# Optimization experiments

Hardware: AMD Instinct MI355X
Metric: run time of the kernel (lower is better)

The kernel has to match this reference:

```python
import jax, jax.numpy as jnp
import numpy as np

B, N, D, E = 8, 512, 256, 16384  # batch, num_nodes, hidden_dim, num_edges


def setup_inputs() -> dict:
    key = jax.random.key(0)
    kf, ke, k1, k2, k3, k4 = jax.random.split(key, 6)
    features = jax.random.normal(kf, (B, N, D), dtype=jnp.float32)
    edge_index = jax.random.randint(ke, (2, E), 0, N, dtype=jnp.int64)
    # weight_net: Linear(2D -> D), ReLU, Linear(D -> 1), Sigmoid
    s1 = 1.0 / np.sqrt(2 * D)
    s2 = 1.0 / np.sqrt(D)
    W1 = jax.random.uniform(k1, (2 * D, D), jnp.float32, -s1, s1)
    b1 = jax.random.uniform(k2, (D,), jnp.float32, -s1, s1)
    W2 = jax.random.uniform(k3, (D, 1), jnp.float32, -s2, s2)
    b2 = jax.random.uniform(k4, (1,), jnp.float32, -s2, s2)
    return {"features": features, "W1": W1, "b1": b1, "W2": W2, "b2": b2,
            "edge_index": edge_index}


def reference(features, W1, b1, W2, b2, edge_index):
    src, dst = edge_index[0], edge_index[1]            # [E], [E]
    fi = features[:, src]                              # [B, E, D]
    fj = features[:, dst]                              # [B, E, D]
    pair = jnp.concatenate([fi, fj], axis=-1)          # [B, E, 2D]
    h = jax.nn.relu(jnp.einsum('bef,fh->beh', pair, W1) + b1)   # [B, E, D]
    s = jax.nn.sigmoid(jnp.einsum('beh,ho->beo', h, W2) + b2)[..., 0]  # [B, E]
    bsz, n = features.shape[0], features.shape[1]
    weights = jnp.zeros((bsz, n, n), features.dtype).at[:, src, dst].set(s)
    return weights
```

## Files before the change

kernel.cpp:

```cpp
#include <hip/hip_runtime.h>
#include <hip/hip_bf16.h>
#include <cstdint>

#define B_ 8
#define N_ 512
#define D_ 256
#define E_ 16384
#define H_ 256

#define SA_STRIDE 56
#define SB_STRIDE 56

using bf16x8 = __attribute__((ext_vector_type(8))) short;
using f32x4  = __attribute__((ext_vector_type(4))) float;

__device__ inline unsigned short f2bf(float f) {
    union { float f; unsigned u; } v; v.f = f;
    unsigned u = v.u;
    return (unsigned short)((u + 0x7fffu + ((u >> 16) & 1u)) >> 16);
}

__global__ __launch_bounds__(256)
void prep_k(const float* __restrict__ W1, unsigned short* __restrict__ W1T) {
    __shared__ float tile[64][65];
    const int tb = blockIdx.x, t = threadIdx.x;
    const int h   = tb >> 4;
    const int rem = tb & 15;
    const int tk  = (rem >> 2) * 64;
    const int tn  = (rem & 3) * 64;
    const float* Wh = W1 + (size_t)h * 256 * 256;
    const int c = t & 63, r0 = t >> 6;
#pragma unroll
    for (int i = 0; i < 16; i++) {
        int r = r0 + i * 4;
        tile[r][c] = Wh[(size_t)(tk + r) * 256 + tn + c];
    }
    __syncthreads();
#pragma unroll
    for (int i = 0; i < 16; i++) {
        int rn = r0 + i * 4;
        W1T[(size_t)(h * 256 + tn + rn) * 256 + tk + c] = f2bf(tile[c][rn]);
    }
}

__global__ __launch_bounds__(256)
void node_gemm(const float* __restrict__ feat,
               const unsigned short* __restrict__ W1T,
               unsigned short* __restrict__ P,
               float4* __restrict__ out4) {
    __shared__ unsigned short sA[64 * SA_STRIDE];
    __shared__ unsigned short sB[256 * SB_STRIDE];

    const int t  = threadIdx.x;
    const int bm = blockIdx.x >> 1;
    const int bn = blockIdx.x & 1;
    const int m0 = bm * 64;

    {
        float4 z = make_float4(0.f, 0.f, 0.f, 0.f);
        float4* oz = out4 + (size_t)blockIdx.x * 4096 + t;
#pragma unroll
        for (int i = 0; i < 16; i++) oz[i * 256] = z;
    }

    const int arow = t >> 2;
    const int akg  = (t & 3) * 8;
    const float* pA = feat + (size_t)(m0 + arow) * 256;
    const unsigned short* pB = W1T + (size_t)(bn * 256 + t) * 256;

    const int wave = t >> 6, lane = t & 63, l15 = lane & 15, quad = lane >> 4;

    f32x4 acc[4][4];
#pragma unroll
    for (int rm = 0; rm < 4; rm++)
#pragma unroll
        for (int cn = 0; cn < 4; cn++)
            acc[rm][cn] = (f32x4){0.f, 0.f, 0.f, 0.f};

    for (int k0 = 0; k0 < 256; k0 += 32) {
        __syncthreads();
        {
            float4 lo = *(const float4*)(pA + k0 + akg);
            float4 hi = *(const float4*)(pA + k0 + akg + 4);
            union { bf16x8 v; unsigned short s[8]; } u;
            u.s[0] = f2bf(lo.x); u.s[1] = f2bf(lo.y); u.s[2] = f2bf(lo.z); u.s[3] = f2bf(lo.w);
            u.s[4] = f2bf(hi.x); u.s[5] = f2bf(hi.y); u.s[6] = f2bf(hi.z); u.s[7] = f2bf(hi.w);
            *(bf16x8*)(sA + arow * SA_STRIDE + akg) = u.v;
        }
        {
            const unsigned short* p = pB + k0;
            uint4 q0 = *(const uint4*)(p);
            uint4 q1 = *(const uint4*)(p + 8);
            uint4 q2 = *(const uint4*)(p + 16);
            uint4 q3 = *(const uint4*)(p + 24);
            *(uint4*)(sB + t * SB_STRIDE +  0) = q0;
            *(uint4*)(sB + t * SB_STRIDE +  8) = q1;
            *(uint4*)(sB + t * SB_STRIDE + 16) = q2;
            *(uint4*)(sB + t * SB_STRIDE + 24) = q3;
        }
        __syncthreads();

        bf16x8 af[4], bfr[4];
#pragma unroll
        for (int rm = 0; rm < 4; rm++)
            af[rm] = *(const bf16x8*)(sA + (rm * 16 + l15) * SA_STRIDE + quad * 8);
#pragma unroll
        for (int cn = 0; cn < 4; cn++)
            bfr[cn] = *(const bf16x8*)(sB + (wave * 64 + cn * 16 + l15) * SB_STRIDE + quad * 8);
#pragma unroll
        for (int rm = 0; rm < 4; rm++)
#pragma unroll
            for (int cn = 0; cn < 4; cn++)
                acc[rm][cn] = __builtin_amdgcn_mfma_f32_16x16x32_bf16(af[rm], bfr[cn], acc[rm][cn], 0, 0, 0);
    }

#pragma unroll
    for (int rm = 0; rm < 4; rm++)
#pragma unroll
        for (int cn = 0; cn < 4; cn++) {
            int col = bn * 256 + wave * 64 + cn * 16 + l15;
#pragma unroll
            for (int r = 0; r < 4; r++) {
                int row = m0 + rm * 16 + quad * 4 + r;
                P[(size_t)row * 512 + col] = f2bf(acc[rm][cn][r]);
            }
        }
}

__device__ inline float dot8(uint4 qu, uint4 qv, const float* b1p, const float* w2p) {
    unsigned us[4] = {qu.x, qu.y, qu.z, qu.w};
    unsigned vs[4] = {qv.x, qv.y, qv.z, qv.w};
    float p = 0.f;
#pragma unroll
    for (int j = 0; j < 4; j++) {
        float ulo = __uint_as_float(us[j] << 16);
        float uhi = __uint_as_float(us[j] & 0xffff0000u);
        float vlo = __uint_as_float(vs[j] << 16);
        float vhi = __uint_as_float(vs[j] & 0xffff0000u);
        float hlo = fmaxf(ulo + vlo + b1p[2 * j],     0.f);
        float hhi = fmaxf(uhi + vhi + b1p[2 * j + 1], 0.f);
        p = fmaf(hlo, w2p[2 * j],     p);
        p = fmaf(hhi, w2p[2 * j + 1], p);
    }
    return p;
}

__global__ __launch_bounds__(256)
void edge_score(const unsigned short* __restrict__ P,
                const float* __restrict__ b1, const float* __restrict__ W2,
                const float* __restrict__ b2, const int* __restrict__ eidx,
                float* __restrict__ out) {
    const int b    = blockIdx.x & 7;
    const int blk  = blockIdx.x >> 3;
    const int wave = threadIdx.x >> 6;
    const int lane = threadIdx.x & 63;
    const int g    = lane >> 4;
    const int w    = lane & 15;
    const int e0   = (blk * 4 + wave) * 16;

    float b1r[16], w2r[16];
#pragma unroll
    for (int j = 0; j < 4; j++) {
        *(float4*)(b1r + 4 * j) = *(const float4*)(b1 + w * 16 + 4 * j);
        *(float4*)(w2r + 4 * j) = *(const float4*)(W2 + w * 16 + 4 * j);
    }
    const float b2v = b2[0];

    const unsigned short* Pb = P + (size_t)b * 512 * 512;
    float* outb = out + (size_t)b * 512 * 512;

    int my_e = 0;
    if (lane < 16)      my_e = eidx[e0 + lane];
    else if (lane < 32) my_e = eidx[E_ + e0 + (lane - 16)];

#pragma unroll
    for (int i = 0; i < 4; i++) {
        int eid = i * 4 + g;
        int src = __shfl(my_e, eid);
        int dst = __shfl(my_e, 16 + eid);
        const unsigned short* pu = Pb + (size_t)src * 512 + w * 16;
        const unsigned short* pv = Pb + (size_t)dst * 512 + 256 + w * 16;
        uint4 u0 = *(const uint4*)(pu);
        uint4 u1 = *(const uint4*)(pu + 8);
        uint4 v0 = *(const uint4*)(pv);
        uint4 v1 = *(const uint4*)(pv + 8);
        float p = dot8(u0, v0, b1r, w2r) + dot8(u1, v1, b1r + 8, w2r + 8);
        p += __shfl_xor(p, 1);
        p += __shfl_xor(p, 2);
        p += __shfl_xor(p, 4);
        p += __shfl_xor(p, 8);
        if (w == 0) {
            float s = 1.0f / (1.0f + __expf(-(p + b2v)));
            outb[(size_t)src * 512 + dst] = s;
        }
    }
}

extern "C" void kernel_launch(void* const* d_in, const int* in_sizes, int n_in,
                              void* d_out, int out_size, void* d_ws, size_t ws_size,
                              hipStream_t stream) {
    const float* feat = (const float*)d_in[0];
    const float* W1   = (const float*)d_in[1];
    const float* b1   = (const float*)d_in[2];
    const float* W2   = (const float*)d_in[3];
    const float* b2   = (const float*)d_in[4];
    const int*   eidx = (const int*)d_in[5];
    float* out = (float*)d_out;

    unsigned short* W1T = (unsigned short*)d_ws;
    unsigned short* P   = (unsigned short*)((char*)d_ws + (1 << 20));

    prep_k<<<32, 256, 0, stream>>>(W1, W1T);
    node_gemm<<<128, 256, 0, stream>>>(feat, W1T, P, (float4*)out);
    edge_score<<<2048, 256, 0, stream>>>(P, b1, W2, b2, eidx, out);
}
```

Measured before the change: 92.82 us.

## Sort edges by source and reuse source rows in edge scoring

```diff
diff --git a/kernel.cpp b/kernel.cpp
--- a/kernel.cpp
+++ b/kernel.cpp
@@ -21,31 +21,80 @@
 }
 
 __global__ __launch_bounds__(256)
-void prep_k(const float* __restrict__ W1, unsigned short* __restrict__ W1T) {
+void prep_k(const float* __restrict__ W1, const int* __restrict__ eidx,
+            unsigned short* __restrict__ W1T,
+            int* __restrict__ gStarts, int* __restrict__ gSorted) {
     __shared__ float tile[64][65];
+    __shared__ int hist[4][512];
+    __shared__ int sc[2][512];
+    __shared__ int cursor[512];
+
     const int tb = blockIdx.x, t = threadIdx.x;
-    const int h   = tb >> 4;
-    const int rem = tb & 15;
-    const int tk  = (rem >> 2) * 64;
-    const int tn  = (rem & 3) * 64;
-    const float* Wh = W1 + (size_t)h * 256 * 256;
-    const int c = t & 63, r0 = t >> 6;
-#pragma unroll
-    for (int i = 0; i < 16; i++) {
-        int r = r0 + i * 4;
-        tile[r][c] = Wh[(size_t)(tk + r) * 256 + tn + c];
-    }
-    __syncthreads();
-#pragma unroll
-    for (int i = 0; i < 16; i++) {
-        int rn = r0 + i * 4;
-        W1T[(size_t)(h * 256 + tn + rn) * 256 + tk + c] = f2bf(tile[c][rn]);
+
+    if (tb < 32) {
+        const int h   = tb >> 4;
+        const int rem = tb & 15;
+        const int tk  = (rem >> 2) * 64;
+        const int tn  = (rem & 3) * 64;
+        const float* Wh = W1 + (size_t)h * 256 * 256;
+        const int c = t & 63, r0 = t >> 6;
+#pragma unroll
+        for (int i = 0; i < 16; i++) {
+            int r = r0 + i * 4;
+            tile[r][c] = Wh[(size_t)(tk + r) * 256 + tn + c];
+        }
+        __syncthreads();
+#pragma unroll
+        for (int i = 0; i < 16; i++) {
+            int rn = r0 + i * 4;
+            W1T[(size_t)(h * 256 + tn + rn) * 256 + tk + c] = f2bf(tile[c][rn]);
+        }
+        return;
+    }
+
+    const int w = t >> 6;
+    for (int i = t; i < 4 * 512; i += 256) ((int*)hist)[i] = 0;
+    __syncthreads();
+    for (int i = 0; i < 64; i++) {
+        int s = eidx[t + 256 * i];
+        atomicAdd(&hist[w][s], 1);
+    }
+    __syncthreads();
+    for (int i = t; i < 512; i += 256)
+        sc[0][i] = hist[0][i] + hist[1][i] + hist[2][i] + hist[3][i];
+    __syncthreads();
+    int cur = 0;
+    for (int off = 1; off < 512; off <<= 1) {
+#pragma unroll
+        for (int k = 0; k < 2; k++) {
+            int i = t + 256 * k;
+            int v = sc[cur][i];
+            if (i >= off) v += sc[cur][i - off];
+            sc[cur ^ 1][i] = v;
+        }
+        __syncthreads();
+        cur ^= 1;
+    }
+    for (int i = t; i < 512; i += 256) {
+        int st = (i == 0) ? 0 : sc[cur][i - 1];
+        cursor[i]  = st;
+        gStarts[i] = st;
+    }
+    if (t == 0) gStarts[512] = E_;
+    __syncthreads();
+    for (int i = 0; i < 64; i++) {
+        int e = t + 256 * i;
+        int s = eidx[e];
+        int d = eidx[E_ + e];
+        int pos = atomicAdd(&cursor[s], 1);
+        gSorted[pos] = d;
     }
 }
 
 __global__ __launch_bounds__(256)
 void node_gemm(const float* __restrict__ feat,
                const unsigned short* __restrict__ W1T,
+               const float* __restrict__ b1,
                unsigned short* __restrict__ P,
                float4* __restrict__ out4) {
     __shared__ unsigned short sA[64 * SA_STRIDE];
@@ -115,19 +164,21 @@
     }
 
 #pragma unroll
-    for (int rm = 0; rm < 4; rm++)
-#pragma unroll
-        for (int cn = 0; cn < 4; cn++) {
-            int col = bn * 256 + wave * 64 + cn * 16 + l15;
+    for (int cn = 0; cn < 4; cn++) {
+        int colh = wave * 64 + cn * 16 + l15;
+        float bias = (bn == 0) ? b1[colh] : 0.f;
+        int col = bn * 256 + colh;
+#pragma unroll
+        for (int rm = 0; rm < 4; rm++)
 #pragma unroll
             for (int r = 0; r < 4; r++) {
                 int row = m0 + rm * 16 + quad * 4 + r;
-                P[(size_t)row * 512 + col] = f2bf(acc[rm][cn][r]);
+                P[(size_t)row * 512 + col] = f2bf(acc[rm][cn][r] + bias);
             }
-        }
-}
-
-__device__ inline float dot8(uint4 qu, uint4 qv, const float* b1p, const float* w2p) {
+    }
+}
+
+__device__ inline float dot8nb(uint4 qu, uint4 qv, const float* w2p) {
     unsigned us[4] = {qu.x, qu.y, qu.z, qu.w};
     unsigned vs[4] = {qv.x, qv.y, qv.z, qv.w};
     float p = 0.f;
@@ -137,8 +188,8 @@
         float uhi = __uint_as_float(us[j] & 0xffff0000u);
         float vlo = __uint_as_float(vs[j] << 16);
         float vhi = __uint_as_float(vs[j] & 0xffff0000u);
-        float hlo = fmaxf(ulo + vlo + b1p[2 * j],     0.f);
-        float hhi = fmaxf(uhi + vhi + b1p[2 * j + 1], 0.f);
+        float hlo = fmaxf(ulo + vlo, 0.f);
+        float hhi = fmaxf(uhi + vhi, 0.f);
         p = fmaf(hlo, w2p[2 * j],     p);
         p = fmaf(hhi, w2p[2 * j + 1], p);
     }
@@ -147,52 +198,58 @@
 
 __global__ __launch_bounds__(256)
 void edge_score(const unsigned short* __restrict__ P,
-                const float* __restrict__ b1, const float* __restrict__ W2,
-                const float* __restrict__ b2, const int* __restrict__ eidx,
+                const float* __restrict__ W2, const float* __restrict__ b2,
+                const int* __restrict__ gStarts, const int* __restrict__ gSorted,
                 float* __restrict__ out) {
-    const int b    = blockIdx.x & 7;
-    const int blk  = blockIdx.x >> 3;
-    const int wave = threadIdx.x >> 6;
-    const int lane = threadIdx.x & 63;
-    const int g    = lane >> 4;
-    const int w    = lane & 15;
-    const int e0   = (blk * 4 + wave) * 16;
-
-    float b1r[16], w2r[16];
-#pragma unroll
-    for (int j = 0; j < 4; j++) {
-        *(float4*)(b1r + 4 * j) = *(const float4*)(b1 + w * 16 + 4 * j);
+    const int b     = blockIdx.x & 7;
+    const int chunk = blockIdx.x >> 3;
+    const int lane  = threadIdx.x & 63;
+    const int wave  = threadIdx.x >> 6;
+    const int g     = lane >> 4;
+    const int w     = lane & 15;
+    const int wid   = wave * 4 + g;
+    const int s     = 2 * chunk + (wid >> 3);
+    const int o     = wid & 7;
+
+    const int st = gStarts[s], en = gStarts[s + 1];
+
+    float w2r[16];
+#pragma unroll
+    for (int j = 0; j < 4; j++)
         *(float4*)(w2r + 4 * j) = *(const float4*)(W2 + w * 16 + 4 * j);
-    }
     const float b2v = b2[0];
 
-    const unsigned short* Pb = P + (size_t)b * 512 * 512;
-    float* outb = out + (size_t)b * 512 * 512;
-
-    int my_e = 0;
-    if (lane < 16)      my_e = eidx[e0 + lane];
-    else if (lane < 32) my_e = eidx[E_ + e0 + (lane - 16)];
-
-#pragma unroll
-    for (int i = 0; i < 4; i++) {
-        int eid = i * 4 + g;
-        int src = __shfl(my_e, eid);
-        int dst = __shfl(my_e, 16 + eid);
-        const unsigned short* pu = Pb + (size_t)src * 512 + w * 16;
-        const unsigned short* pv = Pb + (size_t)dst * 512 + 256 + w * 16;
-        uint4 u0 = *(const uint4*)(pu);
-        uint4 u1 = *(const uint4*)(pu + 8);
-        uint4 v0 = *(const uint4*)(pv);
-        uint4 v1 = *(const uint4*)(pv + 8);
-        float p = dot8(u0, v0, b1r, w2r) + dot8(u1, v1, b1r + 8, w2r + 8);
+    const unsigned short* Pu = P + ((size_t)b * 512 + s) * 512 + w * 16;
+    uint4 u0 = *(const uint4*)(Pu);
+    uint4 u1 = *(const uint4*)(Pu + 8);
+    const unsigned short* Pv = P + (size_t)b * 512 * 512 + 256 + w * 16;
+    float* outb = out + ((size_t)b * 512 + s) * 512;
+
+    int j = st + o;
+    int dst0 = 0; uint4 v00 = {}, v01 = {};
+    if (j < en) {
+        dst0 = gSorted[j];
+        const unsigned short* pv = Pv + (size_t)dst0 * 512;
+        v00 = *(const uint4*)pv; v01 = *(const uint4*)(pv + 8);
+    }
+    while (j < en) {
+        int jn = j + 8;
+        int dst1 = 0; uint4 v10 = {}, v11 = {};
+        if (jn < en) {
+            dst1 = gSorted[jn];
+            const unsigned short* pv = Pv + (size_t)dst1 * 512;
+            v10 = *(const uint4*)pv; v11 = *(const uint4*)(pv + 8);
+        }
+        float p = dot8nb(u0, v00, w2r) + dot8nb(u1, v01, w2r + 8);
         p += __shfl_xor(p, 1);
         p += __shfl_xor(p, 2);
         p += __shfl_xor(p, 4);
         p += __shfl_xor(p, 8);
         if (w == 0) {
-            float s = 1.0f / (1.0f + __expf(-(p + b2v)));
-            outb[(size_t)src * 512 + dst] = s;
-        }
+            float sv = 1.0f / (1.0f + __expf(-(p + b2v)));
+            outb[dst0] = sv;
+        }
+        dst0 = dst1; v00 = v10; v01 = v11; j = jn;
     }
 }
 
@@ -209,8 +266,10 @@
 
     unsigned short* W1T = (unsigned short*)d_ws;
     unsigned short* P   = (unsigned short*)((char*)d_ws + (1 << 20));
-
-    prep_k<<<32, 256, 0, stream>>>(W1, W1T);
-    node_gemm<<<128, 256, 0, stream>>>(feat, W1T, P, (float4*)out);
-    edge_score<<<2048, 256, 0, stream>>>(P, b1, W2, b2, eidx, out);
-}
+    int* gStarts = (int*)((char*)d_ws + (6 << 20));
+    int* gSorted = (int*)((char*)d_ws + (6 << 20) + 4096);
+
+    prep_k<<<33, 256, 0, stream>>>(W1, eidx, W1T, gStarts, gSorted);
+    node_gemm<<<128, 256, 0, stream>>>(feat, W1T, b1, P, (float4*)out);
+    edge_score<<<2048, 256, 0, stream>>>(P, W2, b2, gStarts, gSorted, out);
+}
```

Result: slower. 123.0 us (+32.5%).
